# Kernel optimization log

Hardware: AMD Instinct MI355X
Metric: run time of the kernel (lower is better)

The kernel has to match this reference:

```python
import jax, jax.numpy as jnp
import numpy as np

N_USERS = 50000
N_PRODS = 50000
N_NODES = N_USERS + N_PRODS
N_EDGES = 600000
UD, PD, H, O = 64, 100, 128, 16


def _gcn_conv(x, W, b, src, dst, n):
    """PyG GCNConv: linear transform, add self-loops, sym-normalized scatter-add."""
    x = x @ W                                    # [n, H]
    loop = jnp.arange(n, dtype=src.dtype)
    src = jnp.concatenate([src, loop])
    dst = jnp.concatenate([dst, loop])
    deg = jax.ops.segment_sum(jnp.ones_like(dst, dtype=x.dtype), dst, num_segments=n)
    dinv = jnp.where(deg > 0, jax.lax.rsqrt(deg), 0.0)
    norm = dinv[src] * dinv[dst]                 # [E+n]
    msg = x[src] * norm[:, None]                 # gather + scale
    out = jax.ops.segment_sum(msg, dst, num_segments=n)
    return out + b


def setup_inputs() -> dict:
    key = jax.random.key(0)
    ks = jax.random.split(key, 16)
    s = 0.05
    return {
        "user_feats": jax.random.normal(ks[0], (N_USERS, UD), dtype=jnp.float32),
        "prod_feats": jax.random.normal(ks[1], (N_PRODS, PD), dtype=jnp.float32),
        "edge_index": jax.random.randint(ks[2], (2, N_EDGES), 0, N_NODES, dtype=jnp.int64),
        "Wu": jax.random.normal(ks[3], (UD, H), dtype=jnp.float32) * s,
        "bu": jnp.zeros((H,), dtype=jnp.float32),
        "Wp": jax.random.normal(ks[4], (PD, H), dtype=jnp.float32) * s,
        "bp": jnp.zeros((H,), dtype=jnp.float32),
        "W1": jax.random.normal(ks[5], (H, H), dtype=jnp.float32) * s,
        "b1": jnp.zeros((H,), dtype=jnp.float32),
        "W2": jax.random.normal(ks[6], (H, H), dtype=jnp.float32) * s,
        "b2": jnp.zeros((H,), dtype=jnp.float32),
        "W3": jax.random.normal(ks[7], (H, H), dtype=jnp.float32) * s,
        "b3": jnp.zeros((H,), dtype=jnp.float32),
        "Wo": jax.random.normal(ks[8], (H, O), dtype=jnp.float32) * s,
        "bo": jnp.zeros((O,), dtype=jnp.float32),
    }


def reference(user_feats, prod_feats, edge_index, Wu, bu, Wp, bp,
              W1, b1, W2, b2, W3, b3, Wo, bo):
    src, dst = edge_index[0], edge_index[1]
    user_x = user_feats @ Wu + bu
    prod_x = prod_feats @ Wp + bp
    x = jnp.concatenate([user_x, prod_x], axis=0)   # [N_NODES, H]
    x = jax.nn.relu(_gcn_conv(x, W1, b1, src, dst, N_NODES))
    # dropout p=0.6 is identity in eval mode
    x = jax.nn.relu(_gcn_conv(x, W2, b2, src, dst, N_NODES))
    x = jax.nn.relu(_gcn_conv(x, W3, b3, src, dst, N_NODES))
    return x @ Wo + bo                              # [N_NODES, O]
```

## Files before the change

### kernel.cpp

```cpp
#include <hip/hip_runtime.h>
#include <hip/hip_fp16.h>

#define NU 50000
#define NP 50000
#define NN 100000
#define NE 600000
#define H  128
#define O  16

typedef __attribute__((ext_vector_type(8))) _Float16 half8;
typedef __attribute__((ext_vector_type(4))) _Float16 h4v;
typedef __attribute__((ext_vector_type(4))) float f32x4;

__global__ void k_prep(const float* __restrict__ Wu, const float* __restrict__ Wp,
                       const float* __restrict__ W1, const float* __restrict__ W2,
                       const float* __restrict__ W3, const float* __restrict__ Wo,
                       const float* __restrict__ user, const float* __restrict__ prod,
                       __half* __restrict__ whU, __half* __restrict__ wlU,
                       __half* __restrict__ whP, __half* __restrict__ wlP,
                       __half* __restrict__ wh1, __half* __restrict__ wl1,
                       __half* __restrict__ wh2, __half* __restrict__ wl2,
                       __half* __restrict__ wh3, __half* __restrict__ wl3,
                       __half* __restrict__ whO, __half* __restrict__ wlO,
                       __half* __restrict__ xU, __half* __restrict__ xP,
                       int* __restrict__ cnt, int2* __restrict__ epack) {
    int idx = blockIdx.x * blockDim.x + threadIdx.x;
    if (idx >= 175784) {
        int i = idx - 175784;
        if (i < NU * 16) {
            int e = i * 4;
            float4 v = *(const float4*)(user + e);
            __half2 a = __floats2half2_rn(v.x, v.y);
            __half2 b = __floats2half2_rn(v.z, v.w);
            uint2 o; o.x = *(unsigned*)&a; o.y = *(unsigned*)&b;
            *(uint2*)(xU + e) = o;
        } else {
            int q = i - NU * 16;
            if (q >= NP * 32) return;
            int row = q >> 5, kq = (q & 31) * 4;
            float4 v;
            if (kq < 100) v = *(const float4*)(prod + row * 100 + kq);
            else { v.x = 0.f; v.y = 0.f; v.z = 0.f; v.w = 0.f; }
            __half2 a = __floats2half2_rn(v.x, v.y);
            __half2 b = __floats2half2_rn(v.z, v.w);
            uint2 o; o.x = *(unsigned*)&a; o.y = *(unsigned*)&b;
            *(uint2*)(xP + (size_t)row * 128 + kq) = o;
        }
        return;
    }
    if (idx >= 75776) {
        int i = idx - 75776;
        if (i < NN) cnt[i] = 0;
        else if (i < NN + 8) { int2 z; z.x = 0; z.y = 0; epack[NE + (i - NN)] = z; }
        return;
    }
    const float* W; __half *Wh, *Wl; int K, KPAD, NC;
    if      (idx <  8192) {              W = Wu; Wh = whU; Wl = wlU; K =  64; KPAD =  64; NC = 128; }
    else if (idx < 24576) { idx -=  8192; W = Wp; Wh = whP; Wl = wlP; K = 100; KPAD = 128; NC = 128; }
    else if (idx < 40960) { idx -= 24576; W = W1; Wh = wh1; Wl = wl1; K = 128; KPAD = 128; NC = 128; }
    else if (idx < 57344) { idx -= 40960; W = W2; Wh = wh2; Wl = wl2; K = 128; KPAD = 128; NC = 128; }
    else if (idx < 73728) { idx -= 57344; W = W3; Wh = wh3; Wl = wl3; K = 128; KPAD = 128; NC = 128; }
    else                  { idx -= 73728; W = Wo; Wh = whO; Wl = wlO; K = 128; KPAD = 128; NC =  16; }
    int n = idx / KPAD, k = idx - n * KPAD;
    float x = (k < K) ? W[k * NC + n] * 16.0f : 0.0f;
    __half h = __float2half_rn(x);
    __half l = __float2half_rn(x - __half2float(h));
    Wh[idx] = h; Wl[idx] = l;
}

__global__ void k_count(const int* __restrict__ dst, int* __restrict__ cnt,
                        int* __restrict__ rank, int E) {
    int e = blockIdx.x * blockDim.x + threadIdx.x;
    if (e < E) rank[e] = atomicAdd(&cnt[dst[e]], 1);
}

#define SCAN_TPB 256
#define SCAN_VPT 4
#define SCAN_CHUNK (SCAN_TPB * SCAN_VPT)

__global__ void k_scan1(const int* __restrict__ in, int* __restrict__ out,
                        int* __restrict__ bsums, float* __restrict__ dinv, int n) {
    __shared__ int sh[SCAN_TPB];
    int t = threadIdx.x, b = blockIdx.x;
    int base = b * SCAN_CHUNK + t * SCAN_VPT;
    int v[SCAN_VPT]; int s = 0;
#pragma unroll
    for (int i = 0; i < SCAN_VPT; i++) {
        int idx = base + i;
        v[i] = (idx < n) ? in[idx] : 0;
        if (idx < n) dinv[idx] = rsqrtf((float)(v[i] + 1));
        s += v[i];
    }
    sh[t] = s; __syncthreads();
    for (int off = 1; off < SCAN_TPB; off <<= 1) {
        int x = (t >= off) ? sh[t - off] : 0;
        __syncthreads();
        sh[t] += x;
        __syncthreads();
    }
    int run = (t > 0) ? sh[t - 1] : 0;
    if (t == SCAN_TPB - 1) bsums[b] = sh[t];
#pragma unroll
    for (int i = 0; i < SCAN_VPT; i++) {
        int idx = base + i;
        if (idx < n) out[idx] = run;
        run += v[i];
    }
}

__global__ void k_scan2(int* __restrict__ bsums, int nb) {
    __shared__ int sh[128];
    int t = threadIdx.x;
    int v = (t < nb) ? bsums[t] : 0;
    sh[t] = v; __syncthreads();
    for (int off = 1; off < 128; off <<= 1) {
        int x = (t >= off) ? sh[t - off] : 0;
        __syncthreads();
        sh[t] += x;
        __syncthreads();
    }
    if (t < nb) bsums[t] = sh[t] - v;
}

template <typename AT, int K, int KPAD, int NI, int MI, int NOUT, bool BIAS, bool F32OUT>
__device__ __forceinline__
void gemm_body(const AT* __restrict__ X,
               const __half* __restrict__ Wh, const __half* __restrict__ Wl,
               const float* __restrict__ bias, void* __restrict__ Cout,
               int M, int orow0, int vb) {
    constexpr int KS = KPAD / 32;
    constexpr int CSPLIT = NOUT / (16 * MI);
    const int tid  = threadIdx.x;
    const int wid  = tid >> 6, lane = tid & 63;
    const int lm   = lane & 15, q = lane >> 4;
    const int gw   = vb * 4 + wid;
    const int tile = gw / CSPLIT;
    const int c0   = (gw % CSPLIT) * (MI * 16);
    const int NT   = (M + NI * 16 - 1) / (NI * 16);
    if (tile >= NT) return;
    const int n0 = tile * (NI * 16);

    half8 wh[MI][KS], wl[MI][KS];
#pragma unroll
    for (int mi = 0; mi < MI; mi++)
#pragma unroll
        for (int ks = 0; ks < KS; ks++) {
            const size_t b = (size_t)(c0 + mi * 16 + lm) * KPAD + ks * 32 + q * 8;
            wh[mi][ks] = *(const half8*)&Wh[b];
            wl[mi][ks] = *(const half8*)&Wl[b];
        }

    f32x4 acc[NI][MI];
#pragma unroll
    for (int ni = 0; ni < NI; ni++)
#pragma unroll
        for (int mi = 0; mi < MI; mi++) acc[ni][mi] = (f32x4)0.0f;

#pragma unroll
    for (int ni = 0; ni < NI; ni++) {
        const int node = n0 + ni * 16 + lm;
        half8 xf[KS];
        if (node < M) {
#pragma unroll
            for (int ks = 0; ks < KS; ks++)
                xf[ks] = *(const half8*)((const __half*)X + (size_t)node * KPAD + ks * 32 + q * 8);
        } else {
#pragma unroll
            for (int ks = 0; ks < KS; ks++)
#pragma unroll
                for (int j = 0; j < 8; j++) xf[ks][j] = (_Float16)0.0f;
        }
#pragma unroll
        for (int ks = 0; ks < KS; ks++)
#pragma unroll
            for (int mi = 0; mi < MI; mi++) {
                acc[ni][mi] = __builtin_amdgcn_mfma_f32_16x16x32_f16(wh[mi][ks], xf[ks], acc[ni][mi], 0, 0, 0);
                acc[ni][mi] = __builtin_amdgcn_mfma_f32_16x16x32_f16(wl[mi][ks], xf[ks], acc[ni][mi], 0, 0, 0);
            }
    }

#pragma unroll
    for (int ni = 0; ni < NI; ni++) {
        const int node = n0 + ni * 16 + lm;
        if (node >= M) continue;
#pragma unroll
        for (int mi = 0; mi < MI; mi++) {
            const int cb = c0 + mi * 16 + q * 4;
            float4 bv = BIAS ? *(const float4*)&bias[cb] : make_float4(0.f, 0.f, 0.f, 0.f);
            float v0 = fmaf(acc[ni][mi][0], 0.0625f, bv.x);
            float v1 = fmaf(acc[ni][mi][1], 0.0625f, bv.y);
            float v2 = fmaf(acc[ni][mi][2], 0.0625f, bv.z);
            float v3 = fmaf(acc[ni][mi][3], 0.0625f, bv.w);
            if constexpr (F32OUT) {
                *(float4*)((float*)Cout + (size_t)(orow0 + node) * NOUT + cb) =
                    make_float4(v0, v1, v2, v3);
            } else {
                __half2 h0 = __floats2half2_rn(v0, v1);
                __half2 h1 = __floats2half2_rn(v2, v3);
                uint2 o; o.x = *(unsigned*)&h0; o.y = *(unsigned*)&h1;
                *(uint2*)((__half*)Cout + (size_t)(orow0 + node) * NOUT + cb) = o;
            }
        }
    }
}

template <typename AT, int K, int KPAD, int NI, int MI, int NOUT, bool BIAS, bool F32OUT>
__launch_bounds__(256)
__global__ void k_gemm_reg(const AT* __restrict__ X,
                           const __half* __restrict__ Wh, const __half* __restrict__ Wl,
                           const float* __restrict__ bias, void* __restrict__ Cout,
                           int M, int orow0) {
    gemm_body<AT, K, KPAD, NI, MI, NOUT, BIAS, F32OUT>(X, Wh, Wl, bias, Cout, M, orow0, blockIdx.x);
}

#define BLK_U 782
#define BLK_P 1563
#define BLK_F 2344
__launch_bounds__(256)
__global__ void k_fill_inputs(const int* __restrict__ src, const int* __restrict__ dst,
                              const int* __restrict__ offs, const int* __restrict__ bsums,
                              const int* __restrict__ rank, const float* __restrict__ dinv,
                              int2* __restrict__ epack,
                              const __half* __restrict__ xU, const __half* __restrict__ xP,
                              const __half* __restrict__ whU, const __half* __restrict__ wlU,
                              const __half* __restrict__ whP, const __half* __restrict__ wlP,
                              const float* __restrict__ bu, const float* __restrict__ bp,
                              void* __restrict__ xA) {
    const int b = blockIdx.x;
    if (b < BLK_U) {
        gemm_body<__half,  64,  64, 2, 4, 128, true, false>(xU, whU, wlU, bu, xA, NU, 0, b);
    } else if (b < BLK_U + BLK_P) {
        gemm_body<__half, 128, 128, 2, 2, 128, true, false>(xP, whP, wlP, bp, xA, NP, NU, b - BLK_U);
    } else {
        int e = (b - BLK_U - BLK_P) * 256 + threadIdx.x;
        if (e < NE) {
            int s = src[e], d = dst[e];
            int p = offs[d] + bsums[d >> 10] + rank[e];
            int2 r;
            r.x = s;
            r.y = __float_as_int(dinv[s] * dinv[d]);
            epack[p] = r;
        }
    }
}

__launch_bounds__(256)
__global__ void k_aggregate(const __half* __restrict__ y, const int* __restrict__ offs,
                            const int* __restrict__ bsums, const int2* __restrict__ epack,
                            const float* __restrict__ dinv, const float* __restrict__ bias,
                            __half* __restrict__ out) {
    const int node = __builtin_amdgcn_readfirstlane(blockIdx.x * 4 + (threadIdx.x >> 6));
    const int l = threadIdx.x & 63;
    const int h = l >> 5, j = l & 31;

    int e0 = offs[node] + bsums[node >> 10];
    int e1 = (node + 1 < NN) ? (offs[node + 1] + bsums[(node + 1) >> 10]) : NE;
    e0 = __builtin_amdgcn_readfirstlane(e0);
    e1 = __builtin_amdgcn_readfirstlane(e1);

    const h4v* y4 = (const h4v*)y;

    const float di2 = dinv[node] * dinv[node];
    h4v sv = y4[(size_t)node * 32 + j];
    float4 bv = *(const float4*)&bias[4 * j];

    f32x4 acc0 = (f32x4)0.f, acc1 = (f32x4)0.f, acc2 = (f32x4)0.f, acc3 = (f32x4)0.f;

    for (int e = e0; e < e1; e += 8) {
        const int eb = e + 4 * h;
        const int2* pe = epack + eb;
        int2 p0 = pe[0];
        int2 p1 = pe[1];
        int2 p2 = pe[2];
        int2 p3 = pe[3];
        const bool k0 = (eb + 0 < e1), k1 = (eb + 1 < e1);
        const bool k2 = (eb + 2 < e1), k3 = (eb + 3 < e1);
        float w0 = k0 ? __int_as_float(p0.y) : 0.f;
        float w1 = k1 ? __int_as_float(p1.y) : 0.f;
        float w2 = k2 ? __int_as_float(p2.y) : 0.f;
        float w3 = k3 ? __int_as_float(p3.y) : 0.f;
        const int s0 = k0 ? p0.x : node;
        const int s1 = k1 ? p1.x : node;
        const int s2 = k2 ? p2.x : node;
        const int s3 = k3 ? p3.x : node;
        h4v v0 = y4[(size_t)s0 * 32 + j];
        h4v v1 = y4[(size_t)s1 * 32 + j];
        h4v v2 = y4[(size_t)s2 * 32 + j];
        h4v v3 = y4[(size_t)s3 * 32 + j];
        acc0[0] = fmaf((float)v0[0], w0, acc0[0]); acc0[1] = fmaf((float)v0[1], w0, acc0[1]);
        acc0[2] = fmaf((float)v0[2], w0, acc0[2]); acc0[3] = fmaf((float)v0[3], w0, acc0[3]);
        acc1[0] = fmaf((float)v1[0], w1, acc1[0]); acc1[1] = fmaf((float)v1[1], w1, acc1[1]);
        acc1[2] = fmaf((float)v1[2], w1, acc1[2]); acc1[3] = fmaf((float)v1[3], w1, acc1[3]);
        acc2[0] = fmaf((float)v2[0], w2, acc2[0]); acc2[1] = fmaf((float)v2[1], w2, acc2[1]);
        acc2[2] = fmaf((float)v2[2], w2, acc2[2]); acc2[3] = fmaf((float)v2[3], w2, acc2[3]);
        acc3[0] = fmaf((float)v3[0], w3, acc3[0]); acc3[1] = fmaf((float)v3[1], w3, acc3[1]);
        acc3[2] = fmaf((float)v3[2], w3, acc3[2]); acc3[3] = fmaf((float)v3[3], w3, acc3[3]);
    }

    f32x4 s = (acc0 + acc1) + (acc2 + acc3);
    float t0 = s[0] + __shfl_xor(s[0], 32, 64);
    float t1 = s[1] + __shfl_xor(s[1], 32, 64);
    float t2 = s[2] + __shfl_xor(s[2], 32, 64);
    float t3 = s[3] + __shfl_xor(s[3], 32, 64);

    float r0 = fmaf((float)sv[0], di2, t0) + bv.x;
    float r1 = fmaf((float)sv[1], di2, t1) + bv.y;
    float r2 = fmaf((float)sv[2], di2, t2) + bv.z;
    float r3 = fmaf((float)sv[3], di2, t3) + bv.w;
    if (l < 32) {
        __half2 ha = __floats2half2_rn(fmaxf(r0, 0.f), fmaxf(r1, 0.f));
        __half2 hb = __floats2half2_rn(fmaxf(r2, 0.f), fmaxf(r3, 0.f));
        uint2 o; o.x = *(unsigned*)&ha; o.y = *(unsigned*)&hb;
        *(uint2*)(out + (size_t)node * H + 4 * j) = o;
    }
}

extern "C" void kernel_launch(void* const* d_in, const int* in_sizes, int n_in,
                              void* d_out, int out_size, void* d_ws, size_t ws_size,
                              hipStream_t stream) {
    const float* user = (const float*)d_in[0];
    const float* prod = (const float*)d_in[1];
    const int*   eidx = (const int*)  d_in[2];
    const int*   edst = eidx + NE;
    const int*   esrc = eidx;
    const float* Wu = (const float*)d_in[3];
    const float* bu = (const float*)d_in[4];
    const float* Wp = (const float*)d_in[5];
    const float* bp = (const float*)d_in[6];
    const float* W1 = (const float*)d_in[7];
    const float* b1 = (const float*)d_in[8];
    const float* W2 = (const float*)d_in[9];
    const float* b2 = (const float*)d_in[10];
    const float* W3 = (const float*)d_in[11];
    const float* b3 = (const float*)d_in[12];
    const float* Wo = (const float*)d_in[13];
    const float* bo = (const float*)d_in[14];
    float* out = (float*)d_out;

    char* ws = (char*)d_ws;
    size_t p = 0;
    auto alloc = [&](size_t bytes) -> void* {
        void* r = ws + p;
        p += (bytes + 255) & ~(size_t)255;
        return r;
    };
    __half* xA   = (__half*)alloc((size_t)NN * H * 2);
    __half* xB   = (__half*)alloc((size_t)NN * H * 2);
    __half* xU   = (__half*)alloc((size_t)NU * 64 * 2);
    __half* xP   = (__half*)alloc((size_t)NP * 128 * 2);
    int*   cnt   = (int*)  alloc((size_t)NN * 4);
    int*   rank  = (int*)  alloc((size_t)NE * 4);
    int*   offs  = (int*)  alloc((size_t)(NN + 1) * 4);
    float* dinv  = (float*)alloc((size_t)NN * 4);
    int2*  epack = (int2*) alloc((size_t)(NE + 8) * 8);
    int*   bsums = (int*)  alloc(128 * 4);
    __half* whU = (__half*)alloc(128 * 64 * 2);
    __half* wlU = (__half*)alloc(128 * 64 * 2);
    __half* whP = (__half*)alloc(128 * 128 * 2);
    __half* wlP = (__half*)alloc(128 * 128 * 2);
    __half* wh1 = (__half*)alloc(128 * 128 * 2);
    __half* wl1 = (__half*)alloc(128 * 128 * 2);
    __half* wh2 = (__half*)alloc(128 * 128 * 2);
    __half* wl2 = (__half*)alloc(128 * 128 * 2);
    __half* wh3 = (__half*)alloc(128 * 128 * 2);
    __half* wl3 = (__half*)alloc(128 * 128 * 2);
    __half* whO = (__half*)alloc(16 * 128 * 2);
    __half* wlO = (__half*)alloc(16 * 128 * 2);

    const int NBLK = (NN + SCAN_CHUNK - 1) / SCAN_CHUNK;

    {
        const int total = 175784 + NU * 16 + NP * 32;
        k_prep<<<(total + 255) / 256, 256, 0, stream>>>(
            Wu, Wp, W1, W2, W3, Wo, user, prod,
            whU, wlU, whP, wlP, wh1, wl1, wh2, wl2, wh3, wl3, whO, wlO,
            xU, xP, cnt, epack);
    }

    k_count<<<(NE + 255) / 256, 256, 0, stream>>>(edst, cnt, rank, NE);
    k_scan1<<<NBLK, SCAN_TPB, 0, stream>>>(cnt, offs, bsums, dinv, NN);
    k_scan2<<<1, 128, 0, stream>>>(bsums, NBLK);

    k_fill_inputs<<<BLK_U + BLK_P + BLK_F, 256, 0, stream>>>(
        esrc, edst, offs, bsums, rank, dinv, epack,
        xU, xP, whU, wlU, whP, wlP, bu, bp, xA);

    const int blkG = (1563 * 2 + 3) / 4;
    const int blkO = (1563 + 3) / 4;

    k_gemm_reg<__half, 128, 128, 4, 4, 128, false, false><<<blkG, 256, 0, stream>>>(xA, wh1, wl1, nullptr, xB, NN, 0);
    k_aggregate<<<NN / 4, 256, 0, stream>>>(xB, offs, bsums, epack, dinv, b1, xA);
    k_gemm_reg<__half, 128, 128, 4, 4, 128, false, false><<<blkG, 256, 0, stream>>>(xA, wh2, wl2, nullptr, xB, NN, 0);
    k_aggregate<<<NN / 4, 256, 0, stream>>>(xB, offs, bsums, epack, dinv, b2, xA);
    k_gemm_reg<__half, 128, 128, 4, 4, 128, false, false><<<blkG, 256, 0, stream>>>(xA, wh3, wl3, nullptr, xB, NN, 0);
    k_aggregate<<<NN / 4, 256, 0, stream>>>(xB, offs, bsums, epack, dinv, b3, xA);

    k_gemm_reg<__half, 128, 128, 4, 1, 16, true, true><<<blkO, 256, 0, stream>>>(xA, whO, wlO, bo, out, NN, 0);
}
```

Measured before the change: 291.5 us.

## Fold input projections into first GCN weight to drop one GEMM pass

Precomputes Wu·W1 and Wp·W1 (and the projected biases bu·W1, bp·W1) inside the prep kernel, so the input-projection GEMM writes the layer-1 transformed features directly. This removes the separate 100k×128×128 GEMM for layer 1 and one full read/write of the node-feature buffer. The cost is extra serial dot products in the prep kernel and a different fp16 rounding path, since the intermediate projected features are no longer rounded to half.

Result: faster. 264.0 us (-9.5%).

```diff
diff --git a/kernel.cpp b/kernel.cpp
--- a/kernel.cpp
+++ b/kernel.cpp
@@ -16,17 +16,18 @@
                        const float* __restrict__ W1, const float* __restrict__ W2,
                        const float* __restrict__ W3, const float* __restrict__ Wo,
                        const float* __restrict__ user, const float* __restrict__ prod,
-                       __half* __restrict__ whU, __half* __restrict__ wlU,
-                       __half* __restrict__ whP, __half* __restrict__ wlP,
-                       __half* __restrict__ wh1, __half* __restrict__ wl1,
+                       const float* __restrict__ bu, const float* __restrict__ bp,
+                       __half* __restrict__ whU1, __half* __restrict__ wlU1,
+                       __half* __restrict__ whP1, __half* __restrict__ wlP1,
                        __half* __restrict__ wh2, __half* __restrict__ wl2,
                        __half* __restrict__ wh3, __half* __restrict__ wl3,
                        __half* __restrict__ whO, __half* __restrict__ wlO,
+                       float* __restrict__ bu1, float* __restrict__ bp1,
                        __half* __restrict__ xU, __half* __restrict__ xP,
                        int* __restrict__ cnt, int2* __restrict__ epack) {
     int idx = blockIdx.x * blockDim.x + threadIdx.x;
-    if (idx >= 175784) {
-        int i = idx - 175784;
+    if (idx >= 159656) {
+        int i = idx - 159656;
         if (i < NU * 16) {
             int e = i * 4;
             float4 v = *(const float4*)(user + e);
@@ -48,24 +49,51 @@
         }
         return;
     }
-    if (idx >= 75776) {
-        int i = idx - 75776;
+    if (idx >= 59648) {
+        int i = idx - 59648;
         if (i < NN) cnt[i] = 0;
         else if (i < NN + 8) { int2 z; z.x = 0; z.y = 0; epack[NE + (i - NN)] = z; }
         return;
     }
-    const float* W; __half *Wh, *Wl; int K, KPAD, NC;
-    if      (idx <  8192) {              W = Wu; Wh = whU; Wl = wlU; K =  64; KPAD =  64; NC = 128; }
-    else if (idx < 24576) { idx -=  8192; W = Wp; Wh = whP; Wl = wlP; K = 100; KPAD = 128; NC = 128; }
-    else if (idx < 40960) { idx -= 24576; W = W1; Wh = wh1; Wl = wl1; K = 128; KPAD = 128; NC = 128; }
-    else if (idx < 57344) { idx -= 40960; W = W2; Wh = wh2; Wl = wl2; K = 128; KPAD = 128; NC = 128; }
-    else if (idx < 73728) { idx -= 57344; W = W3; Wh = wh3; Wl = wl3; K = 128; KPAD = 128; NC = 128; }
-    else                  { idx -= 73728; W = Wo; Wh = whO; Wl = wlO; K = 128; KPAD = 128; NC =  16; }
-    int n = idx / KPAD, k = idx - n * KPAD;
-    float x = (k < K) ? W[k * NC + n] * 16.0f : 0.0f;
+    if (idx >= 59392) {
+        int n = idx - 59392;
+        const float* bsrc = (n < 128) ? bu : bp;
+        int nn = n & 127;
+        float acc = 0.f;
+        for (int j = 0; j < 128; ++j) acc = fmaf(bsrc[j], W1[j * 128 + nn], acc);
+        if (n < 128) bu1[nn] = acc; else bp1[nn] = acc;
+        return;
+    }
+    float x;
+    __half *Wh, *Wl; int sidx;
+    if (idx < 8192) {
+        int n = idx >> 6, k = idx & 63;
+        float acc = 0.f;
+        for (int j = 0; j < 128; ++j) acc = fmaf(Wu[k * 128 + j], W1[j * 128 + n], acc);
+        x = acc * 16.0f; Wh = whU1; Wl = wlU1; sidx = idx;
+    } else if (idx < 24576) {
+        int l = idx - 8192;
+        int n = l >> 7, k = l & 127;
+        float acc = 0.f;
+        if (k < 100)
+            for (int j = 0; j < 128; ++j) acc = fmaf(Wp[k * 128 + j], W1[j * 128 + n], acc);
+        x = acc * 16.0f; Wh = whP1; Wl = wlP1; sidx = l;
+    } else if (idx < 40960) {
+        int l = idx - 24576;
+        int n = l >> 7, k = l & 127;
+        x = W2[k * 128 + n] * 16.0f; Wh = wh2; Wl = wl2; sidx = l;
+    } else if (idx < 57344) {
+        int l = idx - 40960;
+        int n = l >> 7, k = l & 127;
+        x = W3[k * 128 + n] * 16.0f; Wh = wh3; Wl = wl3; sidx = l;
+    } else {
+        int l = idx - 57344;
+        int n = l >> 7, k = l & 127;
+        x = Wo[k * 16 + n] * 16.0f; Wh = whO; Wl = wlO; sidx = l;
+    }
     __half h = __float2half_rn(x);
-    __half l = __float2half_rn(x - __half2float(h));
-    Wh[idx] = h; Wl[idx] = l;
+    __half l2 = __float2half_rn(x - __half2float(h));
+    Wh[sidx] = h; Wl[sidx] = l2;
 }
 
 __global__ void k_count(const int* __restrict__ dst, int* __restrict__ cnt,
@@ -217,20 +245,20 @@
 #define BLK_P 1563
 #define BLK_F 2344
 __launch_bounds__(256)
-__global__ void k_fill_inputs(const int* __restrict__ src, const int* __restrict__ dst,
-                              const int* __restrict__ offs, const int* __restrict__ bsums,
-                              const int* __restrict__ rank, const float* __restrict__ dinv,
-                              int2* __restrict__ epack,
-                              const __half* __restrict__ xU, const __half* __restrict__ xP,
-                              const __half* __restrict__ whU, const __half* __restrict__ wlU,
-                              const __half* __restrict__ whP, const __half* __restrict__ wlP,
-                              const float* __restrict__ bu, const float* __restrict__ bp,
-                              void* __restrict__ xA) {
+__global__ void k_fill_g1(const int* __restrict__ src, const int* __restrict__ dst,
+                          const int* __restrict__ offs, const int* __restrict__ bsums,
+                          const int* __restrict__ rank, const float* __restrict__ dinv,
+                          int2* __restrict__ epack,
+                          const __half* __restrict__ xU, const __half* __restrict__ xP,
+                          const __half* __restrict__ whU1, const __half* __restrict__ wlU1,
+                          const __half* __restrict__ whP1, const __half* __restrict__ wlP1,
+                          const float* __restrict__ bu1, const float* __restrict__ bp1,
+                          void* __restrict__ xB) {
     const int b = blockIdx.x;
     if (b < BLK_U) {
-        gemm_body<__half,  64,  64, 2, 4, 128, true, false>(xU, whU, wlU, bu, xA, NU, 0, b);
+        gemm_body<__half,  64,  64, 2, 4, 128, true, false>(xU, whU1, wlU1, bu1, xB, NU, 0, b);
     } else if (b < BLK_U + BLK_P) {
-        gemm_body<__half, 128, 128, 2, 2, 128, true, false>(xP, whP, wlP, bp, xA, NP, NU, b - BLK_U);
+        gemm_body<__half, 128, 128, 2, 2, 128, true, false>(xP, whP1, wlP1, bp1, xB, NP, NU, b - BLK_U);
     } else {
         int e = (b - BLK_U - BLK_P) * 256 + threadIdx.x;
         if (e < NE) {
@@ -354,41 +382,40 @@
     float* dinv  = (float*)alloc((size_t)NN * 4);
     int2*  epack = (int2*) alloc((size_t)(NE + 8) * 8);
     int*   bsums = (int*)  alloc(128 * 4);
-    __half* whU = (__half*)alloc(128 * 64 * 2);
-    __half* wlU = (__half*)alloc(128 * 64 * 2);
-    __half* whP = (__half*)alloc(128 * 128 * 2);
-    __half* wlP = (__half*)alloc(128 * 128 * 2);
-    __half* wh1 = (__half*)alloc(128 * 128 * 2);
-    __half* wl1 = (__half*)alloc(128 * 128 * 2);
+    __half* whU1 = (__half*)alloc(128 * 64 * 2);
+    __half* wlU1 = (__half*)alloc(128 * 64 * 2);
+    __half* whP1 = (__half*)alloc(128 * 128 * 2);
+    __half* wlP1 = (__half*)alloc(128 * 128 * 2);
     __half* wh2 = (__half*)alloc(128 * 128 * 2);
     __half* wl2 = (__half*)alloc(128 * 128 * 2);
     __half* wh3 = (__half*)alloc(128 * 128 * 2);
     __half* wl3 = (__half*)alloc(128 * 128 * 2);
     __half* whO = (__half*)alloc(16 * 128 * 2);
     __half* wlO = (__half*)alloc(16 * 128 * 2);
+    float* bu1  = (float*)alloc(128 * 4);
+    float* bp1  = (float*)alloc(128 * 4);
 
     const int NBLK = (NN + SCAN_CHUNK - 1) / SCAN_CHUNK;
 
     {
-        const int total = 175784 + NU * 16 + NP * 32;
+        const int total = 159656 + NU * 16 + NP * 32;
         k_prep<<<(total + 255) / 256, 256, 0, stream>>>(
-            Wu, Wp, W1, W2, W3, Wo, user, prod,
-            whU, wlU, whP, wlP, wh1, wl1, wh2, wl2, wh3, wl3, whO, wlO,
-            xU, xP, cnt, epack);
+            Wu, Wp, W1, W2, W3, Wo, user, prod, bu, bp,
+            whU1, wlU1, whP1, wlP1, wh2, wl2, wh3, wl3, whO, wlO,
+            bu1, bp1, xU, xP, cnt, epack);
     }
 
     k_count<<<(NE + 255) / 256, 256, 0, stream>>>(edst, cnt, rank, NE);
     k_scan1<<<NBLK, SCAN_TPB, 0, stream>>>(cnt, offs, bsums, dinv, NN);
     k_scan2<<<1, 128, 0, stream>>>(bsums, NBLK);
 
-    k_fill_inputs<<<BLK_U + BLK_P + BLK_F, 256, 0, stream>>>(
+    k_fill_g1<<<BLK_U + BLK_P + BLK_F, 256, 0, stream>>>(
         esrc, edst, offs, bsums, rank, dinv, epack,
-        xU, xP, whU, wlU, whP, wlP, bu, bp, xA);
+        xU, xP, whU1, wlU1, whP1, wlP1, bu1, bp1, xB);
 
     const int blkG = (1563 * 2 + 3) / 4;
     const int blkO = (1563 + 3) / 4;
 
-    k_gemm_reg<__half, 128, 128, 4, 4, 128, false, false><<<blkG, 256, 0, stream>>>(xA, wh1, wl1, nullptr, xB, NN, 0);
     k_aggregate<<<NN / 4, 256, 0, stream>>>(xB, offs, bsums, epack, dinv, b1, xA);
     k_gemm_reg<__half, 128, 128, 4, 4, 128, false, false><<<blkG, 256, 0, stream>>>(xA, wh2, wl2, nullptr, xB, NN, 0);
     k_aggregate<<<NN / 4, 256, 0, stream>>>(xB, offs, bsums, epack, dinv, b2, xA);
```
